# Kernel tuning notes

Hardware: AMD Instinct MI355X
Metric: run time of the kernel (lower is better)

The kernel has to match this reference:

```python
import jax, jax.numpy as jnp
import numpy as np

F = 128          # nbr_fea_len
A = 64           # angle_fea_len
N_EDGES = 100_000
N_ANGLES = 400_000
N_CRYST = 512
EPS = 1e-5
INV_SQRT_2 = 1.0 / 2.0 ** 0.5


def layer_norm(x, g, b):
    mu = jnp.mean(x, axis=-1, keepdims=True)
    var = jnp.var(x, axis=-1, keepdims=True)
    return (x - mu) * jax.lax.rsqrt(var + EPS) * g + b


def setup_inputs() -> dict:
    key = jax.random.key(0)
    ks = jax.random.split(key, 16)
    def lin(k, out_f, in_f):
        return (jax.random.normal(k, (out_f, in_f), jnp.float32) * (1.0 / np.sqrt(in_f))).astype(jnp.float32)
    return {
        "nbr_fea": jax.random.normal(ks[0], (N_EDGES, F), jnp.float32),
        "angle_fea": jax.random.normal(ks[1], (N_ANGLES, A), jnp.float32),
        "angle_nbr_idx": jax.random.randint(ks[2], (N_ANGLES, 2), 0, N_EDGES),
        "crystal_edge_idx": jax.random.randint(ks[3], (N_EDGES,), 0, N_CRYST),
        "crystal_angle_index": jnp.sort(jax.random.randint(ks[4], (N_ANGLES,), 0, N_CRYST)),
        "W_full": lin(ks[5], 2 * F, 2 * F + A),
        "W_mask": lin(ks[6], 1, F),
        "cn_gamma": jnp.ones((2 * F,), jnp.float32),
        "cn_beta": jnp.zeros((2 * F,), jnp.float32),
        "ln_core_g": jnp.ones((F,), jnp.float32),
        "ln_core_b": jnp.zeros((F,), jnp.float32),
        "ln2_g": jnp.ones((F,), jnp.float32),
        "ln2_b": jnp.zeros((F,), jnp.float32),
        "res_W1a": lin(ks[7], F // 2, F), "res_b1a": jnp.zeros((F // 2,), jnp.float32),
        "res_W2a": lin(ks[8], F, F // 2), "res_b2a": jnp.zeros((F,), jnp.float32),
        "res_W1b": lin(ks[9], F // 2, F), "res_b1b": jnp.zeros((F // 2,), jnp.float32),
        "res_W2b": lin(ks[10], F, F // 2), "res_b2b": jnp.zeros((F,), jnp.float32),
    }


def reference(nbr_fea, angle_fea, angle_nbr_idx, crystal_edge_idx, crystal_angle_index,
              W_full, W_mask, cn_gamma, cn_beta, ln_core_g, ln_core_b, ln2_g, ln2_b,
              res_W1a, res_b1a, res_W2a, res_b2a, res_W1b, res_b1b, res_W2b, res_b2b):
    source_idx = angle_nbr_idx[:, 0]
    # gather the two neighbor edge features per angle -> [n_angles, 2F]
    pair = nbr_fea[angle_nbr_idx].reshape(-1, 2 * F)
    total = jnp.concatenate([angle_fea, pair], axis=1)          # [n_angles, 2F+A]
    h = total @ W_full.T                                        # [n_angles, 2F]

    # Crystal_Norm: per-crystal, per-feature normalization over angle rows
    seg = crystal_angle_index
    cnt = jnp.maximum(jax.ops.segment_sum(jnp.ones((h.shape[0], 1), h.dtype), seg, N_CRYST), 1.0)
    mean = jax.ops.segment_sum(h, seg, N_CRYST) / cnt
    diff = h - mean[seg]
    var = jax.ops.segment_sum(diff * diff, seg, N_CRYST) / cnt
    h = diff * jax.lax.rsqrt(var + EPS)[seg] * cn_gamma + cn_beta

    nbr_core, nbr_filter = h[:, :F], h[:, F:]
    nbr_core = jax.nn.silu(layer_norm(nbr_core, ln_core_g, ln_core_b))
    gate = jax.nn.sigmoid(nbr_filter @ W_mask.T)                # [n_angles, 1]
    msg = gate * nbr_core

    # scatter-mean over source edge; empty edges get 0 (matches scatter+pad)
    s = jax.ops.segment_sum(msg, source_idx, N_EDGES)
    c = jax.ops.segment_sum(jnp.ones((msg.shape[0], 1), msg.dtype), source_idx, N_EDGES)
    nbr_sumed = s / jnp.maximum(c, 1.0)

    x = layer_norm(nbr_sumed, ln2_g, ln2_b)
    # two residual bottleneck blocks: x + fc2(silu(fc1(x)))
    x = x + (jax.nn.silu(x @ res_W1a.T + res_b1a) @ res_W2a.T + res_b2a)
    x = x + (jax.nn.silu(x @ res_W1b.T + res_b1b) @ res_W2b.T + res_b2b)
    return INV_SQRT_2 * (nbr_fea + x)
```

## Files before the change

kernel.cpp:

```cpp
#include <hip/hip_runtime.h>
#include <hip/hip_bf16.h>
#include <hip/hip_fp16.h>
#include <cstdint>
#include <cstddef>

#define NF 128
#define N_EDGES 100000
#define N_ANGLES 400000
#define N_CRYST 512
#define KDIM 320
#define TWOF 256
#define EPS_LN 1e-5f
#define INV_SQRT_2 0.70710678118654752440f
#define CAP 32

typedef short short8 __attribute__((ext_vector_type(8)));
typedef float floatx4 __attribute__((ext_vector_type(4)));

__device__ inline unsigned short f2bf(float x) {
    __hip_bfloat16 b = __float2bfloat16(x);
    return *reinterpret_cast<unsigned short*>(&b);
}
__device__ inline float bf2f(__hip_bfloat16 b) { return __bfloat162float(b); }
__device__ inline float bfbits2f(unsigned short u) {
    unsigned int v = ((unsigned int)u) << 16;
    return __uint_as_float(v);
}

__device__ inline uint4 cvt8(float4 a, float4 b) {
    __hip_bfloat162 p0 = __float22bfloat162_rn(make_float2(a.x, a.y));
    __hip_bfloat162 p1 = __float22bfloat162_rn(make_float2(a.z, a.w));
    __hip_bfloat162 p2 = __float22bfloat162_rn(make_float2(b.x, b.y));
    __hip_bfloat162 p3 = __float22bfloat162_rn(make_float2(b.z, b.w));
    uint4 r;
    r.x = *reinterpret_cast<unsigned int*>(&p0);
    r.y = *reinterpret_cast<unsigned int*>(&p1);
    r.z = *reinterpret_cast<unsigned int*>(&p2);
    r.w = *reinterpret_cast<unsigned int*>(&p3);
    return r;
}

__global__ void seg_bounds(const int* __restrict__ seg, int* __restrict__ seg_start) {
    int s = blockIdx.x * blockDim.x + threadIdx.x;
    if (s > N_CRYST) return;
    if (s == N_CRYST) { seg_start[N_CRYST] = N_ANGLES; return; }
    int lo = 0, hi = N_ANGLES;
    while (lo < hi) { int mid = (lo + hi) >> 1; if (seg[mid] < s) lo = mid + 1; else hi = mid; }
    seg_start[s] = lo;
}

__global__ __launch_bounds__(512) void gemm_gather_mfma(
    const float* __restrict__ angle_fea,
    const float* __restrict__ nbr_fea,
    const int*   __restrict__ angle_nbr_idx,
    const float* __restrict__ W_full,
    __hip_bfloat16* __restrict__ hout)
{
    __shared__ uint4 X_lds[512];
    __shared__ uint4 W_lds[1024];

    const int tid  = threadIdx.x;
    const int row0 = blockIdx.x * 128;

    const int xm = tid >> 2;
    const int xk = ((tid & 3) ^ ((xm >> 1) & 3)) * 8;
    const int p0 = angle_nbr_idx[(size_t)(row0 + xm) * 2 + 0];
    const int p1 = angle_nbr_idx[(size_t)(row0 + xm) * 2 + 1];
    int wn[2], wk[2];
    #pragma unroll
    for (int it = 0; it < 2; ++it) {
        int tau = it * 512 + tid;
        wn[it] = tau >> 2;
        wk[it] = ((tau & 3) ^ ((wn[it] >> 1) & 3)) * 8;
    }

    const int wave = tid >> 6, lane = tid & 63;
    const int wrow = (wave & 1) * 64;
    const int wcol = (wave >> 1) * 64;
    const int rl   = lane & 15, kgrp = lane >> 4;
    const int fragoff = (kgrp ^ ((rl >> 1) & 3)) * 16;
    const char* Xb = (const char*)X_lds;
    const char* Wb = (const char*)W_lds;

    floatx4 acc[4][4];
    #pragma unroll
    for (int i = 0; i < 4; ++i)
        #pragma unroll
        for (int j = 0; j < 4; ++j)
            acc[i][j] = (floatx4){0.f, 0.f, 0.f, 0.f};

    float4 xa, xb2, wa0, wb0, wa1, wb1;
    auto loadX = [&](int kbase, float4& a, float4& b) {
        const float* src;
        if (kbase < 64)       src = angle_fea + (size_t)(row0 + xm) * 64 + kbase + xk;
        else if (kbase < 192) src = nbr_fea + (size_t)p0 * 128 + (kbase - 64) + xk;
        else                  src = nbr_fea + (size_t)p1 * 128 + (kbase - 192) + xk;
        a = ((const float4*)src)[0];
        b = ((const float4*)src)[1];
    };
    auto loadW = [&](int kbase, int it, float4& a, float4& b) {
        const float* src = W_full + (size_t)wn[it] * KDIM + kbase + wk[it];
        a = ((const float4*)src)[0];
        b = ((const float4*)src)[1];
    };

    loadX(0, xa, xb2);
    loadW(0, 0, wa0, wb0);
    loadW(0, 1, wa1, wb1);

    #pragma unroll
    for (int kiter = 0; kiter < 10; ++kiter) {
        uint4 xc  = cvt8(xa, xb2);
        uint4 wc0 = cvt8(wa0, wb0);
        uint4 wc1 = cvt8(wa1, wb1);
        if (kiter > 0) __syncthreads();
        X_lds[tid]       = xc;
        W_lds[tid]       = wc0;
        W_lds[512 + tid] = wc1;
        __syncthreads();
        if (kiter < 9) {
            int nb = (kiter + 1) * 32;
            loadX(nb, xa, xb2);
            loadW(nb, 0, wa0, wb0);
            loadW(nb, 1, wa1, wb1);
        }
        short8 wf[4], xf[4];
        #pragma unroll
        for (int i = 0; i < 4; ++i)
            wf[i] = *(const short8*)(Wb + (size_t)(wcol + i * 16 + rl) * 64 + fragoff);
        #pragma unroll
        for (int j = 0; j < 4; ++j)
            xf[j] = *(const short8*)(Xb + (size_t)(wrow + j * 16 + rl) * 64 + fragoff);
        #pragma unroll
        for (int i = 0; i < 4; ++i)
            #pragma unroll
            for (int j = 0; j < 4; ++j)
                acc[i][j] = __builtin_amdgcn_mfma_f32_16x16x32_bf16(wf[i], xf[j], acc[i][j], 0, 0, 0);
    }

    unsigned short* hp = reinterpret_cast<unsigned short*>(hout);
    #pragma unroll
    for (int j = 0; j < 4; ++j) {
        size_t r = (size_t)(row0 + wrow + j * 16 + rl);
        #pragma unroll
        for (int i = 0; i < 4; ++i) {
            int c = wcol + i * 16 + kgrp * 4;
            floatx4 v = acc[i][j];
            uint2 pk;
            pk.x = (unsigned int)f2bf(v[0]) | ((unsigned int)f2bf(v[1]) << 16);
            pk.y = (unsigned int)f2bf(v[2]) | ((unsigned int)f2bf(v[3]) << 16);
            *reinterpret_cast<uint2*>(hp + r * TWOF + c) = pk;
        }
    }
}

__global__ __launch_bounds__(256) void seg_stats(
    const __hip_bfloat16* __restrict__ h,
    const int* __restrict__ seg_start,
    float* __restrict__ segSum, float* __restrict__ segSumSq)
{
    __shared__ float redS[8][256];
    __shared__ float redQ[8][256];
    int seg   = blockIdx.x;
    int split = blockIdx.y;
    int start = seg_start[seg], end = seg_start[seg + 1];
    int n = end - start;
    int g = threadIdx.x >> 5, t = threadIdx.x & 31;
    float s[8] = {0.f,0.f,0.f,0.f,0.f,0.f,0.f,0.f};
    float q[8] = {0.f,0.f,0.f,0.f,0.f,0.f,0.f,0.f};
    if (n > 0) {
        int per = (n + 3) >> 2;
        int r0 = start + split * per;
        int r1 = min(r0 + per, end);
        const unsigned short* hp = (const unsigned short*)h;
        for (int r = r0 + g; r < r1; r += 8) {
            uint4 v = *(const uint4*)(hp + (size_t)r * TWOF + t * 8);
            unsigned int d[4] = {v.x, v.y, v.z, v.w};
            #pragma unroll
            for (int i = 0; i < 4; ++i) {
                float lo = __uint_as_float(d[i] << 16);
                float hi = __uint_as_float(d[i] & 0xffff0000u);
                s[2*i]   += lo; q[2*i]   += lo * lo;
                s[2*i+1] += hi; q[2*i+1] += hi * hi;
            }
        }
    }
    #pragma unroll
    for (int i = 0; i < 8; ++i) { redS[g][t * 8 + i] = s[i]; redQ[g][t * 8 + i] = q[i]; }
    __syncthreads();
    if (n > 0) {
        int col = threadIdx.x;
        float S = 0.f, Q = 0.f;
        #pragma unroll
        for (int gg = 0; gg < 8; ++gg) { S += redS[gg][col]; Q += redQ[gg][col]; }
        atomicAdd(&segSum[seg * TWOF + col], S);
        atomicAdd(&segSumSq[seg * TWOF + col], Q);
    }
}

__global__ __launch_bounds__(256) void seg_finalize(
    const int* __restrict__ seg_start,
    float* __restrict__ segSum, float* __restrict__ segSumSq)
{
    int seg = blockIdx.x;
    int j = threadIdx.x;
    float cnt = (float)max(seg_start[seg + 1] - seg_start[seg], 1);
    float inv = 1.0f / cnt;
    float mean = segSum[seg * TWOF + j] * inv;
    float var  = segSumSq[seg * TWOF + j] * inv - mean * mean;
    segSum[seg * TWOF + j]   = mean;
    segSumSq[seg * TWOF + j] = rsqrtf(var + EPS_LN);
}

__global__ __launch_bounds__(256) void angle_msg(
    __hip_bfloat16* __restrict__ h,
    const int* __restrict__ seg_idx,
    const int* __restrict__ angle_nbr_idx,
    const float* __restrict__ segMean, const float* __restrict__ segScale,
    const float* __restrict__ cn_gamma, const float* __restrict__ cn_beta,
    const float* __restrict__ ln_g, const float* __restrict__ ln_b,
    const float* __restrict__ w_mask,
    int* __restrict__ slot_cnt, int* __restrict__ slots)
{
    int row  = blockIdx.x * 4 + (threadIdx.x >> 6);
    int lane = threadIdx.x & 63;
    int seg  = seg_idx[row];
    int src  = angle_nbr_idx[(size_t)row * 2];

    __hip_bfloat16* hr = h + (size_t)row * TWOF;
    float y[4];
    #pragma unroll
    for (int qq = 0; qq < 4; ++qq) {
        int col = lane + qq * 64;
        float v = bf2f(hr[col]);
        float m = segMean[seg * TWOF + col], sc = segScale[seg * TWOF + col];
        y[qq] = (v - m) * sc * cn_gamma[col] + cn_beta[col];
    }
    float sum = y[0] + y[1], ssq = y[0] * y[0] + y[1] * y[1];
    #pragma unroll
    for (int o = 32; o > 0; o >>= 1) { sum += __shfl_xor(sum, o, 64); ssq += __shfl_xor(ssq, o, 64); }
    float mu  = sum * (1.f / 128.f);
    float var = ssq * (1.f / 128.f) - mu * mu;
    float rs  = rsqrtf(var + EPS_LN);
    float ln0 = (y[0] - mu) * rs * ln_g[lane]      + ln_b[lane];
    float ln1 = (y[1] - mu) * rs * ln_g[lane + 64] + ln_b[lane + 64];
    float si0 = ln0 / (1.f + __expf(-ln0));
    float si1 = ln1 / (1.f + __expf(-ln1));
    float gp = y[2] * w_mask[lane] + y[3] * w_mask[lane + 64];
    #pragma unroll
    for (int o = 32; o > 0; o >>= 1) gp += __shfl_xor(gp, o, 64);
    float gate = 1.f / (1.f + __expf(-gp));

    __half* mrow = reinterpret_cast<__half*>(hr);
    mrow[lane]      = __float2half(gate * si0);
    mrow[lane + 64] = __float2half(gate * si1);

    if (lane == 0) {
        int k = atomicAdd(&slot_cnt[src], 1);
        if (k < CAP) slots[(size_t)src * CAP + k] = row;
    }
}

#define MT 64
#define XBS 136
#define H1S 72
#define W1S 136
#define W2S 72
__global__ __launch_bounds__(256) void edge_mlp_mfma(
    const __hip_bfloat16* __restrict__ hmsg,
    const int* __restrict__ slot_cnt,
    const int* __restrict__ slots,
    const float* __restrict__ nbr_fea,
    const float* __restrict__ ln2_g, const float* __restrict__ ln2_b,
    const float* __restrict__ W1a, const float* __restrict__ b1a,
    const float* __restrict__ W2a, const float* __restrict__ b2a,
    const float* __restrict__ W1b, const float* __restrict__ b1b,
    const float* __restrict__ W2b, const float* __restrict__ b2b,
    float* __restrict__ out)
{
    __shared__ unsigned short xb[MT * XBS];
    __shared__ unsigned short h1[MT * H1S];
    __shared__ unsigned short wl[128 * W2S];

    const int tid  = threadIdx.x;
    const int row0 = blockIdx.x * MT;
    const int w    = tid >> 6, lane = tid & 63;
    const int rl   = lane & 15, kgrp = lane >> 4;

    {
        int m = tid >> 2;
        int q = tid & 3;
        int e = min(row0 + m, N_EDGES - 1);
        int cnt = min(slot_cnt[e], CAP);
        float v[32];
        #pragma unroll
        for (int i = 0; i < 32; ++i) v[i] = 0.f;
        const char* hb = (const char*)hmsg;
        for (int k = 0; k < cnt; ++k) {
            int r = slots[(size_t)e * CAP + k];
            const uint4* mr = (const uint4*)(hb + (size_t)r * 512 + q * 64);
            #pragma unroll
            for (int t = 0; t < 4; ++t) {
                uint4 u = mr[t];
                unsigned int d[4] = {u.x, u.y, u.z, u.w};
                #pragma unroll
                for (int i2 = 0; i2 < 4; ++i2) {
                    __half2 hh = *reinterpret_cast<__half2*>(&d[i2]);
                    float2 f2 = __half22float2(hh);
                    v[8*t + 2*i2]     += f2.x;
                    v[8*t + 2*i2 + 1] += f2.y;
                }
            }
        }
        float inv = 1.f / fmaxf((float)cnt, 1.f);
        float sum = 0.f, ssq = 0.f;
        #pragma unroll
        for (int i = 0; i < 32; ++i) { v[i] *= inv; sum += v[i]; ssq += v[i] * v[i]; }
        sum += __shfl_xor(sum, 1, 64); ssq += __shfl_xor(ssq, 1, 64);
        sum += __shfl_xor(sum, 2, 64); ssq += __shfl_xor(ssq, 2, 64);
        float mu  = sum * (1.f / 128.f);
        float var = ssq * (1.f / 128.f) - mu * mu;
        float rs  = rsqrtf(var + EPS_LN);
        #pragma unroll
        for (int i = 0; i < 32; ++i) {
            int col = q * 32 + i;
            v[i] = (v[i] - mu) * rs * ln2_g[col] + ln2_b[col];
        }
        #pragma unroll
        for (int t = 0; t < 4; ++t) {
            float4 a = make_float4(v[8*t+0], v[8*t+1], v[8*t+2], v[8*t+3]);
            float4 b = make_float4(v[8*t+4], v[8*t+5], v[8*t+6], v[8*t+7]);
            *(uint4*)&xb[m * XBS + q * 32 + t * 8] = cvt8(a, b);
        }
    }

    const float* W1s[2] = {W1a, W1b};
    const float* B1s[2] = {b1a, b1b};
    const float* W2s[2] = {W2a, W2b};
    const float* B2s[2] = {b2a, b2b};

    #pragma unroll 1
    for (int blk = 0; blk < 2; ++blk) {
        const float* W1 = W1s[blk]; const float* B1 = B1s[blk];
        const float* W2 = W2s[blk]; const float* B2 = B2s[blk];

        __syncthreads();
        #pragma unroll
        for (int c = tid; c < 1024; c += 256) {
            int nn = c >> 4, kc = c & 15;
            const float* src = W1 + (size_t)nn * 128 + kc * 8;
            *(uint4*)&wl[nn * W1S + kc * 8] =
                cvt8(((const float4*)src)[0], ((const float4*)src)[1]);
        }
        __syncthreads();

        short8 xf[4];
        #pragma unroll
        for (int ks = 0; ks < 4; ++ks)
            xf[ks] = *(const short8*)&xb[(w * 16 + rl) * XBS + ks * 32 + kgrp * 8];
        floatx4 a1[4];
        #pragma unroll
        for (int i = 0; i < 4; ++i) {
            a1[i] = (floatx4){0.f, 0.f, 0.f, 0.f};
            #pragma unroll
            for (int ks = 0; ks < 4; ++ks) {
                short8 wf = *(const short8*)&wl[(i * 16 + rl) * W1S + ks * 32 + kgrp * 8];
                a1[i] = __builtin_amdgcn_mfma_f32_16x16x32_bf16(wf, xf[ks], a1[i], 0, 0, 0);
            }
        }
        #pragma unroll
        for (int i = 0; i < 4; ++i) {
            int nb = i * 16 + kgrp * 4;
            float s0 = a1[i][0] + B1[nb + 0];
            float s1 = a1[i][1] + B1[nb + 1];
            float s2 = a1[i][2] + B1[nb + 2];
            float s3 = a1[i][3] + B1[nb + 3];
            s0 = s0 / (1.f + __expf(-s0));
            s1 = s1 / (1.f + __expf(-s1));
            s2 = s2 / (1.f + __expf(-s2));
            s3 = s3 / (1.f + __expf(-s3));
            unsigned int lo = (unsigned int)f2bf(s0) | ((unsigned int)f2bf(s1) << 16);
            unsigned int hi = (unsigned int)f2bf(s2) | ((unsigned int)f2bf(s3) << 16);
            *(unsigned int*)&h1[(w * 16 + rl) * H1S + nb]     = lo;
            *(unsigned int*)&h1[(w * 16 + rl) * H1S + nb + 2] = hi;
        }

        __syncthreads();
        #pragma unroll
        for (int c = tid; c < 1024; c += 256) {
            int pp = c >> 3, kc = c & 7;
            const float* src = W2 + (size_t)pp * 64 + kc * 8;
            *(uint4*)&wl[pp * W2S + kc * 8] =
                cvt8(((const float4*)src)[0], ((const float4*)src)[1]);
        }
        __syncthreads();

        short8 hf[2];
        #pragma unroll
        for (int ks = 0; ks < 2; ++ks)
            hf[ks] = *(const short8*)&h1[(w * 16 + rl) * H1S + ks * 32 + kgrp * 8];
        #pragma unroll
        for (int p = 0; p < 8; ++p) {
            floatx4 a2 = (floatx4){0.f, 0.f, 0.f, 0.f};
            #pragma unroll
            for (int ks = 0; ks < 2; ++ks) {
                short8 wf = *(const short8*)&wl[(p * 16 + rl) * W2S + ks * 32 + kgrp * 8];
                a2 = __builtin_amdgcn_mfma_f32_16x16x32_bf16(wf, hf[ks], a2, 0, 0, 0);
            }
            int m = w * 16 + rl;
            #pragma unroll
            for (int reg = 0; reg < 4; ++reg) {
                int pcol = p * 16 + kgrp * 4 + reg;
                int idx  = m * XBS + pcol;
                float xv = bfbits2f(xb[idx]);
                xb[idx] = f2bf(xv + a2[reg] + B2[pcol]);
            }
        }
    }

    {
        int m = tid >> 2;
        int q = tid & 3;
        int e = row0 + m;
        if (e < N_EDGES) {
            const float4* nf = (const float4*)(nbr_fea + (size_t)e * NF + q * 32);
            float4* dst      = (float4*)(out + (size_t)e * NF + q * 32);
            #pragma unroll
            for (int t = 0; t < 8; ++t) {
                float4 f = nf[t];
                int col = q * 32 + 4 * t;
                dst[t] = make_float4(
                    INV_SQRT_2 * (f.x + bfbits2f(xb[m * XBS + col + 0])),
                    INV_SQRT_2 * (f.y + bfbits2f(xb[m * XBS + col + 1])),
                    INV_SQRT_2 * (f.z + bfbits2f(xb[m * XBS + col + 2])),
                    INV_SQRT_2 * (f.w + bfbits2f(xb[m * XBS + col + 3])));
            }
        }
    }
}


extern "C" void kernel_launch(void* const* d_in, const int* in_sizes, int n_in,
                              void* d_out, int out_size, void* d_ws, size_t ws_size,
                              hipStream_t stream) {
    const float* nbr_fea       = (const float*)d_in[0];
    const float* angle_fea     = (const float*)d_in[1];
    const int*   angle_nbr_idx = (const int*)d_in[2];
    const int*   cai           = (const int*)d_in[4];
    const float* W_full        = (const float*)d_in[5];
    const float* W_mask        = (const float*)d_in[6];
    const float* cn_gamma      = (const float*)d_in[7];
    const float* cn_beta       = (const float*)d_in[8];
    const float* ln_core_g     = (const float*)d_in[9];
    const float* ln_core_b     = (const float*)d_in[10];
    const float* ln2_g         = (const float*)d_in[11];
    const float* ln2_b         = (const float*)d_in[12];
    const float* W1a           = (const float*)d_in[13];
    const float* b1a           = (const float*)d_in[14];
    const float* W2a           = (const float*)d_in[15];
    const float* b2a           = (const float*)d_in[16];
    const float* W1b           = (const float*)d_in[17];
    const float* b1b           = (const float*)d_in[18];
    const float* W2b           = (const float*)d_in[19];
    const float* b2b           = (const float*)d_in[20];
    float* out = (float*)d_out;

    char* ws = (char*)d_ws;
    float* segSum    = (float*)(ws + 0);
    float* segSumSq  = (float*)(ws + 524288);
    int*   slot_cnt  = (int*)  (ws + 1048576);
    int*   seg_start = (int*)  (ws + 1448576);
    int*   slots     = (int*)  (ws + 1450752);
    __hip_bfloat16* h = (__hip_bfloat16*)(ws + 14250752);

    hipMemsetAsync(ws, 0, 1448576, stream);

    seg_bounds<<<3, 256, 0, stream>>>(cai, seg_start);
    gemm_gather_mfma<<<N_ANGLES / 128, 512, 0, stream>>>(
        angle_fea, nbr_fea, angle_nbr_idx, W_full, h);
    seg_stats<<<dim3(N_CRYST, 4), 256, 0, stream>>>(h, seg_start, segSum, segSumSq);
    seg_finalize<<<N_CRYST, 256, 0, stream>>>(seg_start, segSum, segSumSq);
    angle_msg<<<N_ANGLES / 4, 256, 0, stream>>>(
        h, cai, angle_nbr_idx, segSum, segSumSq,
        cn_gamma, cn_beta, ln_core_g, ln_core_b, W_mask, slot_cnt, slots);
    edge_mlp_mfma<<<(N_EDGES + MT - 1) / MT, 256, 0, stream>>>(
        h, slot_cnt, slots, nbr_fea, ln2_g, ln2_b,
        W1a, b1a, W2a, b2a, W1b, b1b, W2b, b2b, out);
}
```

Baseline: 666.1 us.

## Fuse per-angle message computation into edge MLP gather and merge finalize into stats

```diff
diff --git a/kernel.cpp b/kernel.cpp
--- a/kernel.cpp
+++ b/kernel.cpp
@@ -21,7 +21,6 @@
     __hip_bfloat16 b = __float2bfloat16(x);
     return *reinterpret_cast<unsigned short*>(&b);
 }
-__device__ inline float bf2f(__hip_bfloat16 b) { return __bfloat162float(b); }
 __device__ inline float bfbits2f(unsigned short u) {
     unsigned int v = ((unsigned int)u) << 16;
     return __uint_as_float(v);
@@ -40,13 +39,27 @@
     return r;
 }
 
-__global__ void seg_bounds(const int* __restrict__ seg, int* __restrict__ seg_start) {
-    int s = blockIdx.x * blockDim.x + threadIdx.x;
-    if (s > N_CRYST) return;
-    if (s == N_CRYST) { seg_start[N_CRYST] = N_ANGLES; return; }
-    int lo = 0, hi = N_ANGLES;
-    while (lo < hi) { int mid = (lo + hi) >> 1; if (seg[mid] < s) lo = mid + 1; else hi = mid; }
-    seg_start[s] = lo;
+__global__ __launch_bounds__(256) void prep(
+    const int* __restrict__ cai,
+    const int* __restrict__ angle_nbr_idx,
+    int* __restrict__ seg_start,
+    int* __restrict__ slot_cnt, int* __restrict__ slots)
+{
+    int gid = blockIdx.x * 256 + threadIdx.x;
+    if (gid <= N_CRYST) {
+        if (gid == N_CRYST) {
+            seg_start[N_CRYST] = N_ANGLES;
+        } else {
+            int lo = 0, hi = N_ANGLES;
+            while (lo < hi) { int mid = (lo + hi) >> 1; if (cai[mid] < gid) lo = mid + 1; else hi = mid; }
+            seg_start[gid] = lo;
+        }
+    }
+    if (gid < N_ANGLES) {
+        int src = angle_nbr_idx[(size_t)gid * 2];
+        int k = atomicAdd(&slot_cnt[src], 1);
+        if (k < CAP) slots[(size_t)src * CAP + k] = gid;
+    }
 }
 
 __global__ __launch_bounds__(512) void gemm_gather_mfma(
@@ -157,10 +170,13 @@
 __global__ __launch_bounds__(256) void seg_stats(
     const __hip_bfloat16* __restrict__ h,
     const int* __restrict__ seg_start,
-    float* __restrict__ segSum, float* __restrict__ segSumSq)
+    const float* __restrict__ cn_gamma, const float* __restrict__ cn_beta,
+    float* __restrict__ segSum, float* __restrict__ segSumSq,
+    int* __restrict__ done)
 {
     __shared__ float redS[8][256];
     __shared__ float redQ[8][256];
+    __shared__ int lastFlag;
     int seg   = blockIdx.x;
     int split = blockIdx.y;
     int start = seg_start[seg], end = seg_start[seg + 1];
@@ -187,6 +203,7 @@
     }
     #pragma unroll
     for (int i = 0; i < 8; ++i) { redS[g][t * 8 + i] = s[i]; redQ[g][t * 8 + i] = q[i]; }
+    if (threadIdx.x == 0) lastFlag = 0;
     __syncthreads();
     if (n > 0) {
         int col = threadIdx.x;
@@ -196,68 +213,26 @@
         atomicAdd(&segSum[seg * TWOF + col], S);
         atomicAdd(&segSumSq[seg * TWOF + col], Q);
     }
-}
-
-__global__ __launch_bounds__(256) void seg_finalize(
-    const int* __restrict__ seg_start,
-    float* __restrict__ segSum, float* __restrict__ segSumSq)
-{
-    int seg = blockIdx.x;
-    int j = threadIdx.x;
-    float cnt = (float)max(seg_start[seg + 1] - seg_start[seg], 1);
-    float inv = 1.0f / cnt;
-    float mean = segSum[seg * TWOF + j] * inv;
-    float var  = segSumSq[seg * TWOF + j] * inv - mean * mean;
-    segSum[seg * TWOF + j]   = mean;
-    segSumSq[seg * TWOF + j] = rsqrtf(var + EPS_LN);
-}
-
-__global__ __launch_bounds__(256) void angle_msg(
-    __hip_bfloat16* __restrict__ h,
-    const int* __restrict__ seg_idx,
-    const int* __restrict__ angle_nbr_idx,
-    const float* __restrict__ segMean, const float* __restrict__ segScale,
-    const float* __restrict__ cn_gamma, const float* __restrict__ cn_beta,
-    const float* __restrict__ ln_g, const float* __restrict__ ln_b,
-    const float* __restrict__ w_mask,
-    int* __restrict__ slot_cnt, int* __restrict__ slots)
-{
-    int row  = blockIdx.x * 4 + (threadIdx.x >> 6);
-    int lane = threadIdx.x & 63;
-    int seg  = seg_idx[row];
-    int src  = angle_nbr_idx[(size_t)row * 2];
-
-    __hip_bfloat16* hr = h + (size_t)row * TWOF;
-    float y[4];
-    #pragma unroll
-    for (int qq = 0; qq < 4; ++qq) {
-        int col = lane + qq * 64;
-        float v = bf2f(hr[col]);
-        float m = segMean[seg * TWOF + col], sc = segScale[seg * TWOF + col];
-        y[qq] = (v - m) * sc * cn_gamma[col] + cn_beta[col];
-    }
-    float sum = y[0] + y[1], ssq = y[0] * y[0] + y[1] * y[1];
-    #pragma unroll
-    for (int o = 32; o > 0; o >>= 1) { sum += __shfl_xor(sum, o, 64); ssq += __shfl_xor(ssq, o, 64); }
-    float mu  = sum * (1.f / 128.f);
-    float var = ssq * (1.f / 128.f) - mu * mu;
-    float rs  = rsqrtf(var + EPS_LN);
-    float ln0 = (y[0] - mu) * rs * ln_g[lane]      + ln_b[lane];
-    float ln1 = (y[1] - mu) * rs * ln_g[lane + 64] + ln_b[lane + 64];
-    float si0 = ln0 / (1.f + __expf(-ln0));
-    float si1 = ln1 / (1.f + __expf(-ln1));
-    float gp = y[2] * w_mask[lane] + y[3] * w_mask[lane + 64];
-    #pragma unroll
-    for (int o = 32; o > 0; o >>= 1) gp += __shfl_xor(gp, o, 64);
-    float gate = 1.f / (1.f + __expf(-gp));
-
-    __half* mrow = reinterpret_cast<__half*>(hr);
-    mrow[lane]      = __float2half(gate * si0);
-    mrow[lane + 64] = __float2half(gate * si1);
-
-    if (lane == 0) {
-        int k = atomicAdd(&slot_cnt[src], 1);
-        if (k < CAP) slots[(size_t)src * CAP + k] = row;
+    __syncthreads();
+    if (n > 0 && threadIdx.x == 0) {
+        __threadfence();
+        int old = atomicAdd(&done[seg], 1);
+        if (old == 3) lastFlag = 1;
+    }
+    __syncthreads();
+    if (lastFlag) {
+        int j = threadIdx.x;
+        float S = atomicAdd(&segSum[seg * TWOF + j], 0.0f);
+        float Q = atomicAdd(&segSumSq[seg * TWOF + j], 0.0f);
+        float cnt = (float)max(n, 1);
+        float inv = 1.0f / cnt;
+        float mean = S * inv;
+        float var  = Q * inv - mean * mean;
+        float rs   = rsqrtf(var + EPS_LN);
+        float A = rs * cn_gamma[j];
+        float B = cn_beta[j] - mean * A;
+        segSum[seg * TWOF + j]   = A;
+        segSumSq[seg * TWOF + j] = B;
     }
 }
 
@@ -267,10 +242,14 @@
 #define W1S 136
 #define W2S 72
 __global__ __launch_bounds__(256) void edge_mlp_mfma(
-    const __hip_bfloat16* __restrict__ hmsg,
+    const __hip_bfloat16* __restrict__ h,
+    const int* __restrict__ cai,
     const int* __restrict__ slot_cnt,
     const int* __restrict__ slots,
+    const float* __restrict__ segA, const float* __restrict__ segB,
     const float* __restrict__ nbr_fea,
+    const float* __restrict__ lncg, const float* __restrict__ lncb,
+    const float* __restrict__ w_mask,
     const float* __restrict__ ln2_g, const float* __restrict__ ln2_b,
     const float* __restrict__ W1a, const float* __restrict__ b1a,
     const float* __restrict__ W2a, const float* __restrict__ b2a,
@@ -286,52 +265,78 @@
     const int row0 = blockIdx.x * MT;
     const int w    = tid >> 6, lane = tid & 63;
     const int rl   = lane & 15, kgrp = lane >> 4;
-
-    {
-        int m = tid >> 2;
-        int q = tid & 3;
-        int e = min(row0 + m, N_EDGES - 1);
-        int cnt = min(slot_cnt[e], CAP);
-        float v[32];
-        #pragma unroll
-        for (int i = 0; i < 32; ++i) v[i] = 0.f;
-        const char* hb = (const char*)hmsg;
+    const int c0   = 2 * lane;
+
+    const float g0  = lncg[c0],  g1  = lncg[c0 + 1];
+    const float lb0 = lncb[c0],  lb1 = lncb[c0 + 1];
+    const float wm0 = w_mask[c0], wm1 = w_mask[c0 + 1];
+    const float l2g0 = ln2_g[c0], l2g1 = ln2_g[c0 + 1];
+    const float l2b0 = ln2_b[c0], l2b1 = ln2_b[c0 + 1];
+
+    for (int i = 0; i < 16; ++i) {
+        const int m = w * 16 + i;
+        const int e = row0 + m;
+        float acc0 = 0.f, acc1 = 0.f;
+        int cnt = 0;
+        if (e < N_EDGES) cnt = min(slot_cnt[e], CAP);
+        int rN = 0, segN = 0;
+        if (cnt > 0) {
+            rN   = slots[(size_t)e * CAP];
+            segN = cai[rN];
+        }
         for (int k = 0; k < cnt; ++k) {
-            int r = slots[(size_t)e * CAP + k];
-            const uint4* mr = (const uint4*)(hb + (size_t)r * 512 + q * 64);
-            #pragma unroll
-            for (int t = 0; t < 4; ++t) {
-                uint4 u = mr[t];
-                unsigned int d[4] = {u.x, u.y, u.z, u.w};
-                #pragma unroll
-                for (int i2 = 0; i2 < 4; ++i2) {
-                    __half2 hh = *reinterpret_cast<__half2*>(&d[i2]);
-                    float2 f2 = __half22float2(hh);
-                    v[8*t + 2*i2]     += f2.x;
-                    v[8*t + 2*i2 + 1] += f2.y;
-                }
-            }
+            const int r = rN, seg = segN;
+            if (k + 1 < cnt) {
+                rN   = slots[(size_t)e * CAP + k + 1];
+                segN = cai[rN];
+            }
+            const unsigned int* hrow = (const unsigned int*)(h + (size_t)r * TWOF);
+            const unsigned int uc = hrow[lane];
+            const unsigned int uf = hrow[64 + lane];
+            const float* As = segA + (size_t)seg * TWOF;
+            const float* Bs = segB + (size_t)seg * TWOF;
+            const float2 A0 = *(const float2*)(As + c0);
+            const float2 B0 = *(const float2*)(Bs + c0);
+            const float2 A1 = *(const float2*)(As + 128 + c0);
+            const float2 B1 = *(const float2*)(Bs + 128 + c0);
+            float y0 = bfbits2f((unsigned short)(uc & 0xffffu)) * A0.x + B0.x;
+            float y1 = bfbits2f((unsigned short)(uc >> 16))     * A0.y + B0.y;
+            float f0 = bfbits2f((unsigned short)(uf & 0xffffu)) * A1.x + B1.x;
+            float f1 = bfbits2f((unsigned short)(uf >> 16))     * A1.y + B1.y;
+            float sum = y0 + y1;
+            float ssq = y0 * y0 + y1 * y1;
+            float gp  = f0 * wm0 + f1 * wm1;
+            #pragma unroll
+            for (int o = 32; o > 0; o >>= 1) {
+                sum += __shfl_xor(sum, o, 64);
+                ssq += __shfl_xor(ssq, o, 64);
+                gp  += __shfl_xor(gp,  o, 64);
+            }
+            float mu   = sum * (1.f / 128.f);
+            float var  = ssq * (1.f / 128.f) - mu * mu;
+            float rs   = rsqrtf(var + EPS_LN);
+            float gate = 1.f / (1.f + __expf(-gp));
+            float ln0 = (y0 - mu) * rs * g0 + lb0;
+            float ln1 = (y1 - mu) * rs * g1 + lb1;
+            acc0 += gate * (ln0 / (1.f + __expf(-ln0)));
+            acc1 += gate * (ln1 / (1.f + __expf(-ln1)));
         }
         float inv = 1.f / fmaxf((float)cnt, 1.f);
-        float sum = 0.f, ssq = 0.f;
-        #pragma unroll
-        for (int i = 0; i < 32; ++i) { v[i] *= inv; sum += v[i]; ssq += v[i] * v[i]; }
-        sum += __shfl_xor(sum, 1, 64); ssq += __shfl_xor(ssq, 1, 64);
-        sum += __shfl_xor(sum, 2, 64); ssq += __shfl_xor(ssq, 2, 64);
+        acc0 *= inv; acc1 *= inv;
+        float sum = acc0 + acc1;
+        float ssq = acc0 * acc0 + acc1 * acc1;
+        #pragma unroll
+        for (int o = 32; o > 0; o >>= 1) {
+            sum += __shfl_xor(sum, o, 64);
+            ssq += __shfl_xor(ssq, o, 64);
+        }
         float mu  = sum * (1.f / 128.f);
         float var = ssq * (1.f / 128.f) - mu * mu;
         float rs  = rsqrtf(var + EPS_LN);
-        #pragma unroll
-        for (int i = 0; i < 32; ++i) {
-            int col = q * 32 + i;
-            v[i] = (v[i] - mu) * rs * ln2_g[col] + ln2_b[col];
-        }
-        #pragma unroll
-        for (int t = 0; t < 4; ++t) {
-            float4 a = make_float4(v[8*t+0], v[8*t+1], v[8*t+2], v[8*t+3]);
-            float4 b = make_float4(v[8*t+4], v[8*t+5], v[8*t+6], v[8*t+7]);
-            *(uint4*)&xb[m * XBS + q * 32 + t * 8] = cvt8(a, b);
-        }
+        float x0 = (acc0 - mu) * rs * l2g0 + l2b0;
+        float x1 = (acc1 - mu) * rs * l2g1 + l2b1;
+        __hip_bfloat162 p = __float22bfloat162_rn(make_float2(x0, x1));
+        *(unsigned int*)&xb[m * XBS + c0] = *reinterpret_cast<unsigned int*>(&p);
     }
 
     const float* W1s[2] = {W1a, W1b};
@@ -469,21 +474,21 @@
     float* segSum    = (float*)(ws + 0);
     float* segSumSq  = (float*)(ws + 524288);
     int*   slot_cnt  = (int*)  (ws + 1048576);
-    int*   seg_start = (int*)  (ws + 1448576);
-    int*   slots     = (int*)  (ws + 1450752);
-    __hip_bfloat16* h = (__hip_bfloat16*)(ws + 14250752);
-
-    hipMemsetAsync(ws, 0, 1448576, stream);
-
-    seg_bounds<<<3, 256, 0, stream>>>(cai, seg_start);
+    int*   done      = (int*)  (ws + 1448576);
+    int*   seg_start = (int*)  (ws + 1450624);
+    int*   slots     = (int*)  (ws + 1452800);
+    __hip_bfloat16* h = (__hip_bfloat16*)(ws + 14252800);
+
+    hipMemsetAsync(ws, 0, 1450624, stream);
+
+    prep<<<(N_ANGLES + 255) / 256, 256, 0, stream>>>(
+        cai, angle_nbr_idx, seg_start, slot_cnt, slots);
     gemm_gather_mfma<<<N_ANGLES / 128, 512, 0, stream>>>(
         angle_fea, nbr_fea, angle_nbr_idx, W_full, h);
-    seg_stats<<<dim3(N_CRYST, 4), 256, 0, stream>>>(h, seg_start, segSum, segSumSq);
-    seg_finalize<<<N_CRYST, 256, 0, stream>>>(seg_start, segSum, segSumSq);
-    angle_msg<<<N_ANGLES / 4, 256, 0, stream>>>(
-        h, cai, angle_nbr_idx, segSum, segSumSq,
-        cn_gamma, cn_beta, ln_core_g, ln_core_b, W_mask, slot_cnt, slots);
+    seg_stats<<<dim3(N_CRYST, 4), 256, 0, stream>>>(
+        h, seg_start, cn_gamma, cn_beta, segSum, segSumSq, done);
     edge_mlp_mfma<<<(N_EDGES + MT - 1) / MT, 256, 0, stream>>>(
-        h, slot_cnt, slots, nbr_fea, ln2_g, ln2_b,
+        h, cai, slot_cnt, slots, segSum, segSumSq, nbr_fea,
+        ln_core_g, ln_core_b, W_mask, ln2_g, ln2_b,
         W1a, b1a, W2a, b2a, W1b, b1b, W2b, b2b, out);
 }
```

After: 849.9 us. 27.6% more time.
